# Optimization experiments

Hardware: AMD Instinct MI355X
Metric: run time of the kernel (lower is better)

The kernel has to match this reference:

```python
import jax, jax.numpy as jnp
import numpy as np

PAIRS = np.array([[0, 4], [1, 5], [2, 6], [3, 7], [0, 5], [1, 4], [2, 7], [3, 6]])


def setup_inputs() -> dict:
    key = jax.random.key(0)
    ks = jax.random.split(key, 40)
    rn = lambda k, shape: (jax.random.normal(k, shape, jnp.float32) * 0.05)
    inp = {
        "waiting": jax.random.uniform(ks[0], (1, 8), jnp.float32),
        "phase": jax.random.uniform(ks[1], (1, 8), jnp.float32),
        "wtime_mu": jax.random.uniform(ks[2], (1, 8), jnp.float32),
        "wtime_sigma": jax.random.uniform(ks[3], (1, 8), jnp.float32),
        "wtime_max": jax.random.uniform(ks[4], (1, 8), jnp.float32),
        "i_position": jax.random.uniform(ks[5], (1, 1), jnp.float32),
        "j_position": jax.random.uniform(ks[6], (1, 1), jnp.float32),
        # NN_demand: 14 -> 256 -> 32 -> 4
        "d_w1": rn(ks[7], (256, 14)), "d_b1": rn(ks[8], (256,)),
        "d_w2": rn(ks[9], (32, 256)), "d_b2": rn(ks[10], (32,)),
        "d_w3": rn(ks[11], (4, 32)), "d_b3": rn(ks[12], (4,)),
        # NN_coupled_demand: 8 -> 128 -> 32 -> 4
        "c_w1": rn(ks[13], (128, 8)), "c_b1": rn(ks[14], (128,)),
        "c_w2": rn(ks[15], (32, 128)), "c_b2": rn(ks[16], (32,)),
        "c_w3": rn(ks[17], (4, 32)), "c_b3": rn(ks[18], (4,)),
        # Conv_D: 1x1 convs 8 -> 256 -> 32 -> 2
        "dD_w1": rn(ks[19], (256, 8)), "dD_b1": rn(ks[20], (256,)),
        "dD_w2": rn(ks[21], (32, 256)), "dD_b2": rn(ks[22], (32,)),
        "dD_w3": rn(ks[23], (2, 32)), "dD_b3": rn(ks[24], (2,)),
        # Conv_C: 1x1 convs 3 -> 256 -> 32 -> 8, then (1,7) conv 8 -> 1
        "cC_w1": rn(ks[25], (256, 3)), "cC_b1": rn(ks[26], (256,)),
        "cC_w2": rn(ks[27], (32, 256)), "cC_b2": rn(ks[28], (32,)),
        "cC_w3": rn(ks[29], (8, 32)), "cC_b3": rn(ks[30], (8,)),
        "cC_w4": rn(ks[31], (8, 7)), "cC_b4": rn(ks[32], (1,)),
    }
    return inp


def _mlp3(x, w1, b1, w2, b2, w3, b3):
    h = jax.nn.relu(x @ w1.T + b1)
    h = jax.nn.relu(h @ w2.T + b2)
    return h @ w3.T + b3


def _frap_forward(waiting, phase, wtime_mu, wtime_sigma, wtime_max, i_position, j_position,
                  d_w1, d_b1, d_w2, d_b2, d_w3, d_b3,
                  c_w1, c_b1, c_w2, c_b2, c_w3, c_b3,
                  dD_w1, dD_b1, dD_w2, dD_b2, dD_w3, dD_b3,
                  cC_w1, cC_b1, cC_w2, cC_b2, cC_w3, cC_b3, cC_w4, cC_b4):
    pairs = jnp.asarray(PAIRS)
    # per-lane demand features: (8, 14) = [i, j, mu_l, sigma_l, max_l, wait_l, phase(8)]
    feat = jnp.concatenate([
        jnp.broadcast_to(i_position[0], (8, 1)),
        jnp.broadcast_to(j_position[0], (8, 1)),
        wtime_mu[0, :, None], wtime_sigma[0, :, None],
        wtime_max[0, :, None], waiting[0, :, None],
        jnp.broadcast_to(phase[0][None, :], (8, 8)),
    ], axis=1)
    demand = _mlp3(feat, d_w1, d_b1, d_w2, d_b2, d_w3, d_b3)  # (8, 4)
    # coupled demand per phase pair: (8, 8) -> (8, 4)
    vec = jnp.concatenate([demand[pairs[:, 0]], demand[pairs[:, 1]]], axis=1)
    dp = _mlp3(vec, c_w1, c_b1, c_w2, c_b2, c_w3, c_b3)  # (8, 4)
    # D tensor (8, 8, 7): D[0:4, i, k] = dp[i]; D[4:8, i, k] = dp[j(k)], j(k)=k + (k>=i)
    k = jnp.arange(7)
    i = jnp.arange(8)
    j_idx = k[None, :] + (k[None, :] >= i[:, None]).astype(jnp.int32)  # (8, 7)
    top = jnp.broadcast_to(dp.T[:, :, None], (4, 8, 7))
    bot = jnp.transpose(dp[j_idx], (2, 0, 1))  # (4, 8, 7)
    D = jnp.concatenate([top, bot], axis=0)  # (8, 8, 7)
    # Conv_D: 1x1 convs are channel matmuls on (C, H, W)
    h = jax.nn.relu(jnp.einsum('oc,chw->ohw', dD_w1, D) + dD_b1[:, None, None])
    h = jax.nn.relu(jnp.einsum('oc,chw->ohw', dD_w2, h) + dD_b2[:, None, None])
    H_d = jnp.einsum('oc,chw->ohw', dD_w3, h) + dD_b3[:, None, None]  # (2, 8, 7)
    comp = jnp.zeros((1, 8, 7), H_d.dtype)
    H_c = jnp.concatenate([H_d, comp], axis=0)  # (3, 8, 7)
    # Conv_C
    h = jax.nn.relu(jnp.einsum('oc,chw->ohw', cC_w1, H_c) + cC_b1[:, None, None])
    h = jax.nn.relu(jnp.einsum('oc,chw->ohw', cC_w2, h) + cC_b2[:, None, None])
    h = jax.nn.relu(jnp.einsum('oc,chw->ohw', cC_w3, h) + cC_b3[:, None, None])  # (8, 8, 7)
    # conv4: kernel (1,7), out (1, 8, 1); return C[0, :, 0] -> (8,)
    out = jnp.einsum('cw,chw->h', cC_w4, h) + cC_b4[0]
    return out


def reference(waiting, phase, wtime_mu, wtime_sigma, wtime_max, i_position, j_position,
              d_w1, d_b1, d_w2, d_b2, d_w3, d_b3,
              c_w1, c_b1, c_w2, c_b2, c_w3, c_b3,
              dD_w1, dD_b1, dD_w2, dD_b2, dD_w3, dD_b3,
              cC_w1, cC_b1, cC_w2, cC_b2, cC_w3, cC_b3, cC_w4, cC_b4):
    return _frap_forward(waiting, phase, wtime_mu, wtime_sigma, wtime_max, i_position, j_position,
                         d_w1, d_b1, d_w2, d_b2, d_w3, d_b3,
                         c_w1, c_b1, c_w2, c_b2, c_w3, c_b3,
                         dD_w1, dD_b1, dD_w2, dD_b2, dD_w3, dD_b3,
                         cC_w1, cC_b1, cC_w2, cC_b2, cC_w3, cC_b3, cC_w4, cC_b4)
```

## Files before the change

### kernel.cpp

```cpp
#include <hip/hip_runtime.h>


#define DEV __device__ __forceinline__

#define WAVE_SYNC() do { \
    asm volatile("s_waitcnt lgkmcnt(0)" ::: "memory"); \
    __builtin_amdgcn_sched_barrier(0); \
} while (0)

DEV float dot4a(float acc, float4 a, float4 b) {
    acc = fmaf(a.x, b.x, acc);
    acc = fmaf(a.y, b.y, acc);
    acc = fmaf(a.z, b.z, acc);
    acc = fmaf(a.w, b.w, acc);
    return acc;
}

DEV float warm_arr(const float* __restrict__ p, int n4, int id, float sink) {
    const float4* p4 = (const float4*)p;
    for (int i = id; i < n4; i += 448) {
        float4 v = p4[i];
        sink += v.x + v.y + v.z + v.w;
    }
    return sink;
}

DEV void conv_h2_vec(const float* __restrict__ big, const float* __restrict__ w2g,
                     const float* __restrict__ b2g, float* __restrict__ mid, int t)
{
    int wv = t >> 6;
    int ln = t & 63;
    int sl = ln & 15;
    int ch = wv * 4 + (ln >> 4);
    if (sl < 14) {
        const float4* wp = (const float4*)(w2g + ch * 256);
        const float* hrow = big + (sl << 8);
        int sw = sl & 7;
        float a0 = 0.0f, a1 = 0.0f, a2 = 0.0f, a3 = 0.0f;
#pragma unroll 4
        for (int g = 0; g < 64; g += 4) {
            float4 w0 = wp[g + 0], w1 = wp[g + 1], w2 = wp[g + 2], w3 = wp[g + 3];
            float4 h0 = *(const float4*)(hrow + (((g + 0) ^ sw) << 2));
            float4 h1 = *(const float4*)(hrow + (((g + 1) ^ sw) << 2));
            float4 h2 = *(const float4*)(hrow + (((g + 2) ^ sw) << 2));
            float4 h3v = *(const float4*)(hrow + (((g + 3) ^ sw) << 2));
            a0 = dot4a(a0, h0, w0);
            a1 = dot4a(a1, h1, w1);
            a2 = dot4a(a2, h2, w2);
            a3 = dot4a(a3, h3v, w3);
        }
        float r = ((a0 + a1) + (a2 + a3)) + b2g[ch];
        mid[ch * 14 + sl] = fmaxf(r, 0.0f);
    }
}

__global__ __launch_bounds__(512, 1) void frap_kernel(
    const float* __restrict__ waiting, const float* __restrict__ phase,
    const float* __restrict__ wtime_mu, const float* __restrict__ wtime_sigma,
    const float* __restrict__ wtime_max,
    const float* __restrict__ i_pos, const float* __restrict__ j_pos,
    const float* __restrict__ d_w1, const float* __restrict__ d_b1,
    const float* __restrict__ d_w2, const float* __restrict__ d_b2,
    const float* __restrict__ d_w3, const float* __restrict__ d_b3,
    const float* __restrict__ c_w1, const float* __restrict__ c_b1,
    const float* __restrict__ c_w2, const float* __restrict__ c_b2,
    const float* __restrict__ c_w3, const float* __restrict__ c_b3,
    const float* __restrict__ dD_w1, const float* __restrict__ dD_b1,
    const float* __restrict__ dD_w2, const float* __restrict__ dD_b2,
    const float* __restrict__ dD_w3, const float* __restrict__ dD_b3,
    const float* __restrict__ cC_w1, const float* __restrict__ cC_b1,
    const float* __restrict__ cC_w2, const float* __restrict__ cC_b2,
    const float* __restrict__ cC_w3, const float* __restrict__ cC_b3,
    const float* __restrict__ cC_w4, const float* __restrict__ cC_b4,
    float* __restrict__ out)
{
    __shared__ __align__(16) float sm[4096];
    const int t  = threadIdx.x;
    const int wg = blockIdx.x;
    const int ln = t & 63;

    float* feat16 = sm;
    float* dh1  = sm + 128;
    float* dh2  = sm + 2176;
    float* dem  = sm + 2432;
    float* ch1  = sm + 2464;
    float* ch2  = sm + 3488;
    float* big  = sm;
    float* mid  = sm + 3584;
    float* dp   = sm + 4032;
    float* Hd   = sm + 4064;
    float* h3   = sm;

    if (t < 64) {
        for (int rep = 0; rep < 2; ++rep) {
            int idx = rep * 64 + ln;
            int l = idx >> 4, c = idx & 15;
            float v = 0.0f;
            if      (c == 0) v = i_pos[0];
            else if (c == 1) v = j_pos[0];
            else if (c == 2) v = wtime_mu[l];
            else if (c == 3) v = wtime_sigma[l];
            else if (c == 4) v = wtime_max[l];
            else if (c == 5) v = waiting[l];
            else if (c < 14) v = phase[c - 6];
            feat16[idx] = v;
        }
        WAVE_SYNC();

        for (int q = 0; q < 4; ++q) {
            int o = q * 64 + ln;
            const float* w = d_w1 + o * 14;
            float w0 = w[0], w1 = w[1], w2 = w[2], w3 = w[3], w4 = w[4];
            float w5 = w[5], w6 = w[6], w7 = w[7], w8 = w[8], w9 = w[9];
            float wa = w[10], wb = w[11], wc = w[12], wd = w[13];
            float bias = d_b1[o];
#pragma unroll
            for (int l = 0; l < 8; ++l) {
                const float4* f4 = (const float4*)(feat16 + l * 16);
                float4 f0 = f4[0], f1 = f4[1], f2 = f4[2], f3 = f4[3];
                float acc = bias;
                acc = fmaf(f0.x, w0, acc); acc = fmaf(f0.y, w1, acc);
                acc = fmaf(f0.z, w2, acc); acc = fmaf(f0.w, w3, acc);
                acc = fmaf(f1.x, w4, acc); acc = fmaf(f1.y, w5, acc);
                acc = fmaf(f1.z, w6, acc); acc = fmaf(f1.w, w7, acc);
                acc = fmaf(f2.x, w8, acc); acc = fmaf(f2.y, w9, acc);
                acc = fmaf(f2.z, wa, acc); acc = fmaf(f2.w, wb, acc);
                acc = fmaf(f3.x, wc, acc); acc = fmaf(f3.y, wd, acc);
                dh1[l * 256 + o] = fmaxf(acc, 0.0f);
            }
        }
        WAVE_SYNC();

        {
            int o = ln & 31, lh = ln >> 5;
            float acc0 = 0.0f, acc1 = 0.0f, acc2 = 0.0f, acc3 = 0.0f;
            const float4* w4p = (const float4*)(d_w2 + o * 256);
#pragma unroll 4
            for (int cb = 0; cb < 64; ++cb) {
                float4 w = w4p[cb];
                float4 h0 = *(const float4*)(dh1 + (lh * 4 + 0) * 256 + cb * 4);
                float4 h1 = *(const float4*)(dh1 + (lh * 4 + 1) * 256 + cb * 4);
                float4 h2 = *(const float4*)(dh1 + (lh * 4 + 2) * 256 + cb * 4);
                float4 h3v = *(const float4*)(dh1 + (lh * 4 + 3) * 256 + cb * 4);
                acc0 = dot4a(acc0, h0, w);
                acc1 = dot4a(acc1, h1, w);
                acc2 = dot4a(acc2, h2, w);
                acc3 = dot4a(acc3, h3v, w);
            }
            float b = d_b2[o];
            dh2[(lh * 4 + 0) * 32 + o] = fmaxf(acc0 + b, 0.0f);
            dh2[(lh * 4 + 1) * 32 + o] = fmaxf(acc1 + b, 0.0f);
            dh2[(lh * 4 + 2) * 32 + o] = fmaxf(acc2 + b, 0.0f);
            dh2[(lh * 4 + 3) * 32 + o] = fmaxf(acc3 + b, 0.0f);
        }
        WAVE_SYNC();

        if (ln < 32) {
            int l = ln >> 2, o = ln & 3;
            const float4* w = (const float4*)(d_w3 + o * 32);
            const float4* h = (const float4*)(dh2 + l * 32);
            float acc = d_b3[o];
#pragma unroll
            for (int g = 0; g < 8; ++g) acc = dot4a(acc, h[g], w[g]);
            dem[ln] = acc;
        }
        WAVE_SYNC();

        for (int rep = 0; rep < 2; ++rep) {
            int o = rep * 64 + ln;
            const float4* w = (const float4*)(c_w1 + o * 8);
            float4 w0 = w[0], w1 = w[1];
            float bias = c_b1[o];
#pragma unroll
            for (int p = 0; p < 8; ++p) {
                int a0 = p & 3;
                int a1 = (p < 4) ? (4 + (p & 3)) : (4 + ((p & 3) ^ 1));
                float4 va = *(const float4*)(dem + a0 * 4);
                float4 vb = *(const float4*)(dem + a1 * 4);
                float acc = dot4a(dot4a(bias, va, w0), vb, w1);
                ch1[p * 128 + o] = fmaxf(acc, 0.0f);
            }
        }
        WAVE_SYNC();

        {
            int o = ln & 31, lh = ln >> 5;
            float acc0 = 0.0f, acc1 = 0.0f, acc2 = 0.0f, acc3 = 0.0f;
            const float4* w4p = (const float4*)(c_w2 + o * 128);
#pragma unroll 4
            for (int cb = 0; cb < 32; ++cb) {
                float4 w = w4p[cb];
                float4 h0 = *(const float4*)(ch1 + (lh * 4 + 0) * 128 + cb * 4);
                float4 h1 = *(const float4*)(ch1 + (lh * 4 + 1) * 128 + cb * 4);
                float4 h2 = *(const float4*)(ch1 + (lh * 4 + 2) * 128 + cb * 4);
                float4 h3v = *(const float4*)(ch1 + (lh * 4 + 3) * 128 + cb * 4);
                acc0 = dot4a(acc0, h0, w);
                acc1 = dot4a(acc1, h1, w);
                acc2 = dot4a(acc2, h2, w);
                acc3 = dot4a(acc3, h3v, w);
            }
            float b = c_b2[o];
            ch2[(lh * 4 + 0) * 32 + o] = fmaxf(acc0 + b, 0.0f);
            ch2[(lh * 4 + 1) * 32 + o] = fmaxf(acc1 + b, 0.0f);
            ch2[(lh * 4 + 2) * 32 + o] = fmaxf(acc2 + b, 0.0f);
            ch2[(lh * 4 + 3) * 32 + o] = fmaxf(acc3 + b, 0.0f);
        }
        WAVE_SYNC();

        if (ln < 32) {
            int l = ln >> 2, o = ln & 3;
            const float4* w = (const float4*)(c_w3 + o * 32);
            const float4* h = (const float4*)(ch2 + l * 32);
            float acc = c_b3[o];
#pragma unroll
            for (int g = 0; g < 8; ++g) acc = dot4a(acc, h[g], w[g]);
            dp[ln] = acc;
        }
    } else {
        int id = t - 64;
        float snk = 0.0f;
        snk = warm_arr(d_w1,  896, id, snk);
        snk = warm_arr(d_b1,   64, id, snk);
        snk = warm_arr(d_w2, 2048, id, snk);
        snk = warm_arr(d_b2,    8, id, snk);
        snk = warm_arr(d_w3,   32, id, snk);
        snk = warm_arr(d_b3,    1, id, snk);
        snk = warm_arr(c_w1,  256, id, snk);
        snk = warm_arr(c_b1,   32, id, snk);
        snk = warm_arr(c_w2, 1024, id, snk);
        snk = warm_arr(c_b2,    8, id, snk);
        snk = warm_arr(c_w3,   32, id, snk);
        snk = warm_arr(c_b3,    1, id, snk);
        snk = warm_arr(dD_w1, 512, id, snk);
        snk = warm_arr(dD_b1,  64, id, snk);
        snk = warm_arr(dD_w2, 2048, id, snk);
        snk = warm_arr(dD_b2,   8, id, snk);
        snk = warm_arr(dD_w3,  16, id, snk);
        snk = warm_arr(cC_w1, 192, id, snk);
        snk = warm_arr(cC_b1,  64, id, snk);
        snk = warm_arr(cC_w2, 2048, id, snk);
        snk = warm_arr(cC_b2,   8, id, snk);
        snk = warm_arr(cC_w3,  64, id, snk);
        snk = warm_arr(cC_b3,   2, id, snk);
        snk = warm_arr(cC_w4,  14, id, snk);
        asm volatile("" :: "v"(snk));
    }
    __syncthreads();

    {
        const float4* dp4 = (const float4*)dp;
        int o = t & 255;
        const float4* wrow = (const float4*)(dD_w1 + o * 8);
        float4 w0 = wrow[0], w1 = wrow[1];
        float bias = dD_b1[o];
#pragma unroll
        for (int it = 0; it < 7; ++it) {
            int sl = (t >> 8) + it * 2;
            int sg = wg * 14 + sl;
            int i = sg / 7, k = sg - i * 7;
            int j = k + (k >= i ? 1 : 0);
            float acc = dot4a(dot4a(bias, dp4[i], w0), dp4[j], w1);
            big[(sl << 8) + (o ^ ((sl & 7) << 2))] = fmaxf(acc, 0.0f);
        }
    }
    __syncthreads();

    conv_h2_vec(big, dD_w2, dD_b2, mid, t);
    __syncthreads();

    if (t < 112) {
        int kq = t & 3, u = t >> 2;
        int o = (u >= 14) ? 1 : 0;
        int s = u - o * 14;
        float acc = 0.0f;
#pragma unroll
        for (int cc = 0; cc < 8; ++cc) {
            int c = kq * 8 + cc;
            acc = fmaf(mid[c * 14 + s], dD_w3[o * 32 + c], acc);
        }
        acc += __shfl_xor(acc, 1);
        acc += __shfl_xor(acc, 2);
        if (kq == 0) Hd[o * 14 + s] = acc + dD_b3[o];
    }
    __syncthreads();

    {
        int o = t & 255;
        float w0 = cC_w1[o * 3], w1 = cC_w1[o * 3 + 1];
        float bias = cC_b1[o];
#pragma unroll
        for (int it = 0; it < 7; ++it) {
            int sl = (t >> 8) + it * 2;
            float acc = fmaf(Hd[14 + sl], w1, fmaf(Hd[sl], w0, bias));
            big[(sl << 8) + (o ^ ((sl & 7) << 2))] = fmaxf(acc, 0.0f);
        }
    }
    __syncthreads();

    conv_h2_vec(big, cC_w2, cC_b2, mid, t);
    __syncthreads();

    if (t < 448) {
        int kq = t & 3, u = t >> 2;
        int o = u & 7, s = u >> 3;
        float acc = 0.0f;
#pragma unroll
        for (int cc = 0; cc < 8; ++cc) {
            int c = kq * 8 + cc;
            acc = fmaf(mid[c * 14 + s], cC_w3[o * 32 + c], acc);
        }
        acc += __shfl_xor(acc, 1);
        acc += __shfl_xor(acc, 2);
        if (kq == 0) h3[o * 14 + s] = fmaxf(acc + cC_b3[o], 0.0f);
    }
    __syncthreads();

    if (t < 16) {
        int r = t >> 3, c = t & 7;
        float p = 0.0f;
#pragma unroll
        for (int w = 0; w < 7; ++w)
            p = fmaf(cC_w4[c * 7 + w], h3[c * 14 + r * 7 + w], p);
#pragma unroll
        for (int off = 1; off < 8; off <<= 1) p += __shfl_xor(p, off);
        if (c == 0) out[wg * 2 + r] = p + cC_b4[0];
    }
}

extern "C" void kernel_launch(void* const* d_in, const int* in_sizes, int n_in,
                              void* d_out, int out_size, void* d_ws, size_t ws_size,
                              hipStream_t stream) {
    (void)in_sizes; (void)n_in; (void)d_ws; (void)ws_size; (void)out_size;
    const float* a[33];
    for (int i = 0; i < 33; ++i) a[i] = (const float*)d_in[i];
    frap_kernel<<<dim3(4), dim3(512), 0, stream>>>(
        a[0], a[1], a[2], a[3], a[4], a[5], a[6],
        a[7], a[8], a[9], a[10], a[11], a[12],
        a[13], a[14], a[15], a[16], a[17], a[18],
        a[19], a[20], a[21], a[22], a[23], a[24],
        a[25], a[26], a[27], a[28], a[29], a[30], a[31], a[32],
        (float*)d_out);
}
```

Measured before the change: 27.88 us.

## Split work across eight blocks and spread demand MLP over all threads

The grid goes from 4 to 8 workgroups, so each block computes one output row of 7 spatial positions instead of two rows of 14. The first two layers of the demand MLP, which a single wave used to run, are now spread over all 512 threads using split-K with shuffle reductions. The conv layer-2 routine is also rewritten with a two-way K split. This cuts the serial single-wave prologue and the per-block conv work, at the cost of extra block-wide barriers and the redundant prologue running in twice as many blocks.

```diff
diff --git a/kernel.cpp b/kernel.cpp
--- a/kernel.cpp
+++ b/kernel.cpp
@@ -28,30 +28,31 @@
 DEV void conv_h2_vec(const float* __restrict__ big, const float* __restrict__ w2g,
                      const float* __restrict__ b2g, float* __restrict__ mid, int t)
 {
-    int wv = t >> 6;
-    int ln = t & 63;
-    int sl = ln & 15;
-    int ch = wv * 4 + (ln >> 4);
-    if (sl < 14) {
-        const float4* wp = (const float4*)(w2g + ch * 256);
+    int kq = t & 1;
+    int u  = t >> 1;
+    int ch = u >> 3, sl = u & 7;
+    float a0 = 0.0f, a1 = 0.0f, a2 = 0.0f, a3 = 0.0f;
+    if (sl < 7) {
+        const float4* wp = (const float4*)(w2g + ch * 256) + kq * 32;
         const float* hrow = big + (sl << 8);
-        int sw = sl & 7;
-        float a0 = 0.0f, a1 = 0.0f, a2 = 0.0f, a3 = 0.0f;
-#pragma unroll 4
-        for (int g = 0; g < 64; g += 4) {
+#pragma unroll 2
+        for (int g = 0; g < 32; g += 4) {
+            int gg = kq * 32 + g;
             float4 w0 = wp[g + 0], w1 = wp[g + 1], w2 = wp[g + 2], w3 = wp[g + 3];
-            float4 h0 = *(const float4*)(hrow + (((g + 0) ^ sw) << 2));
-            float4 h1 = *(const float4*)(hrow + (((g + 1) ^ sw) << 2));
-            float4 h2 = *(const float4*)(hrow + (((g + 2) ^ sw) << 2));
-            float4 h3v = *(const float4*)(hrow + (((g + 3) ^ sw) << 2));
+            float4 h0 = *(const float4*)(hrow + (((gg + 0) ^ sl) << 2));
+            float4 h1 = *(const float4*)(hrow + (((gg + 1) ^ sl) << 2));
+            float4 h2 = *(const float4*)(hrow + (((gg + 2) ^ sl) << 2));
+            float4 h3v = *(const float4*)(hrow + (((gg + 3) ^ sl) << 2));
             a0 = dot4a(a0, h0, w0);
             a1 = dot4a(a1, h1, w1);
             a2 = dot4a(a2, h2, w2);
             a3 = dot4a(a3, h3v, w3);
         }
-        float r = ((a0 + a1) + (a2 + a3)) + b2g[ch];
-        mid[ch * 14 + sl] = fmaxf(r, 0.0f);
-    }
+    }
+    float r = (a0 + a1) + (a2 + a3);
+    r += __shfl_xor(r, 1);
+    if (sl < 7 && kq == 0)
+        mid[ch * 7 + sl] = fmaxf(r + b2g[ch], 0.0f);
 }
 
 __global__ __launch_bounds__(512, 1) void frap_kernel(
@@ -86,9 +87,9 @@
     float* ch1  = sm + 2464;
     float* ch2  = sm + 3488;
     float* big  = sm;
-    float* mid  = sm + 3584;
-    float* dp   = sm + 4032;
-    float* Hd   = sm + 4064;
+    float* mid  = sm + 3744;
+    float* dp   = sm + 3968;
+    float* Hd   = sm + 4000;
     float* h3   = sm;
 
     if (t < 64) {
@@ -104,117 +105,6 @@
             else if (c == 5) v = waiting[l];
             else if (c < 14) v = phase[c - 6];
             feat16[idx] = v;
-        }
-        WAVE_SYNC();
-
-        for (int q = 0; q < 4; ++q) {
-            int o = q * 64 + ln;
-            const float* w = d_w1 + o * 14;
-            float w0 = w[0], w1 = w[1], w2 = w[2], w3 = w[3], w4 = w[4];
-            float w5 = w[5], w6 = w[6], w7 = w[7], w8 = w[8], w9 = w[9];
-            float wa = w[10], wb = w[11], wc = w[12], wd = w[13];
-            float bias = d_b1[o];
-#pragma unroll
-            for (int l = 0; l < 8; ++l) {
-                const float4* f4 = (const float4*)(feat16 + l * 16);
-                float4 f0 = f4[0], f1 = f4[1], f2 = f4[2], f3 = f4[3];
-                float acc = bias;
-                acc = fmaf(f0.x, w0, acc); acc = fmaf(f0.y, w1, acc);
-                acc = fmaf(f0.z, w2, acc); acc = fmaf(f0.w, w3, acc);
-                acc = fmaf(f1.x, w4, acc); acc = fmaf(f1.y, w5, acc);
-                acc = fmaf(f1.z, w6, acc); acc = fmaf(f1.w, w7, acc);
-                acc = fmaf(f2.x, w8, acc); acc = fmaf(f2.y, w9, acc);
-                acc = fmaf(f2.z, wa, acc); acc = fmaf(f2.w, wb, acc);
-                acc = fmaf(f3.x, wc, acc); acc = fmaf(f3.y, wd, acc);
-                dh1[l * 256 + o] = fmaxf(acc, 0.0f);
-            }
-        }
-        WAVE_SYNC();
-
-        {
-            int o = ln & 31, lh = ln >> 5;
-            float acc0 = 0.0f, acc1 = 0.0f, acc2 = 0.0f, acc3 = 0.0f;
-            const float4* w4p = (const float4*)(d_w2 + o * 256);
-#pragma unroll 4
-            for (int cb = 0; cb < 64; ++cb) {
-                float4 w = w4p[cb];
-                float4 h0 = *(const float4*)(dh1 + (lh * 4 + 0) * 256 + cb * 4);
-                float4 h1 = *(const float4*)(dh1 + (lh * 4 + 1) * 256 + cb * 4);
-                float4 h2 = *(const float4*)(dh1 + (lh * 4 + 2) * 256 + cb * 4);
-                float4 h3v = *(const float4*)(dh1 + (lh * 4 + 3) * 256 + cb * 4);
-                acc0 = dot4a(acc0, h0, w);
-                acc1 = dot4a(acc1, h1, w);
-                acc2 = dot4a(acc2, h2, w);
-                acc3 = dot4a(acc3, h3v, w);
-            }
-            float b = d_b2[o];
-            dh2[(lh * 4 + 0) * 32 + o] = fmaxf(acc0 + b, 0.0f);
-            dh2[(lh * 4 + 1) * 32 + o] = fmaxf(acc1 + b, 0.0f);
-            dh2[(lh * 4 + 2) * 32 + o] = fmaxf(acc2 + b, 0.0f);
-            dh2[(lh * 4 + 3) * 32 + o] = fmaxf(acc3 + b, 0.0f);
-        }
-        WAVE_SYNC();
-
-        if (ln < 32) {
-            int l = ln >> 2, o = ln & 3;
-            const float4* w = (const float4*)(d_w3 + o * 32);
-            const float4* h = (const float4*)(dh2 + l * 32);
-            float acc = d_b3[o];
-#pragma unroll
-            for (int g = 0; g < 8; ++g) acc = dot4a(acc, h[g], w[g]);
-            dem[ln] = acc;
-        }
-        WAVE_SYNC();
-
-        for (int rep = 0; rep < 2; ++rep) {
-            int o = rep * 64 + ln;
-            const float4* w = (const float4*)(c_w1 + o * 8);
-            float4 w0 = w[0], w1 = w[1];
-            float bias = c_b1[o];
-#pragma unroll
-            for (int p = 0; p < 8; ++p) {
-                int a0 = p & 3;
-                int a1 = (p < 4) ? (4 + (p & 3)) : (4 + ((p & 3) ^ 1));
-                float4 va = *(const float4*)(dem + a0 * 4);
-                float4 vb = *(const float4*)(dem + a1 * 4);
-                float acc = dot4a(dot4a(bias, va, w0), vb, w1);
-                ch1[p * 128 + o] = fmaxf(acc, 0.0f);
-            }
-        }
-        WAVE_SYNC();
-
-        {
-            int o = ln & 31, lh = ln >> 5;
-            float acc0 = 0.0f, acc1 = 0.0f, acc2 = 0.0f, acc3 = 0.0f;
-            const float4* w4p = (const float4*)(c_w2 + o * 128);
-#pragma unroll 4
-            for (int cb = 0; cb < 32; ++cb) {
-                float4 w = w4p[cb];
-                float4 h0 = *(const float4*)(ch1 + (lh * 4 + 0) * 128 + cb * 4);
-                float4 h1 = *(const float4*)(ch1 + (lh * 4 + 1) * 128 + cb * 4);
-                float4 h2 = *(const float4*)(ch1 + (lh * 4 + 2) * 128 + cb * 4);
-                float4 h3v = *(const float4*)(ch1 + (lh * 4 + 3) * 128 + cb * 4);
-                acc0 = dot4a(acc0, h0, w);
-                acc1 = dot4a(acc1, h1, w);
-                acc2 = dot4a(acc2, h2, w);
-                acc3 = dot4a(acc3, h3v, w);
-            }
-            float b = c_b2[o];
-            ch2[(lh * 4 + 0) * 32 + o] = fmaxf(acc0 + b, 0.0f);
-            ch2[(lh * 4 + 1) * 32 + o] = fmaxf(acc1 + b, 0.0f);
-            ch2[(lh * 4 + 2) * 32 + o] = fmaxf(acc2 + b, 0.0f);
-            ch2[(lh * 4 + 3) * 32 + o] = fmaxf(acc3 + b, 0.0f);
-        }
-        WAVE_SYNC();
-
-        if (ln < 32) {
-            int l = ln >> 2, o = ln & 3;
-            const float4* w = (const float4*)(c_w3 + o * 32);
-            const float4* h = (const float4*)(ch2 + l * 32);
-            float acc = c_b3[o];
-#pragma unroll
-            for (int g = 0; g < 8; ++g) acc = dot4a(acc, h[g], w[g]);
-            dp[ln] = acc;
         }
     } else {
         int id = t - 64;
@@ -247,20 +137,112 @@
     }
     __syncthreads();
 
+    for (int q = 0; q < 4; ++q) {
+        int idx = t + q * 512;
+        int l = idx >> 8, o = idx & 255;
+        const float* w = d_w1 + o * 14;
+        const float* f = feat16 + l * 16;
+        float acc = d_b1[o];
+#pragma unroll
+        for (int c = 0; c < 14; ++c) acc = fmaf(f[c], w[c], acc);
+        dh1[idx] = fmaxf(acc, 0.0f);
+    }
+    __syncthreads();
+
+    {
+        int kq = t & 1;
+        int u  = t >> 1;
+        int l = u >> 5, o = u & 31;
+        const float4* w = (const float4*)(d_w2 + o * 256) + kq * 32;
+        const float4* h = (const float4*)(dh1 + l * 256) + kq * 32;
+        float acc = 0.0f;
+#pragma unroll 4
+        for (int g = 0; g < 32; ++g) acc = dot4a(acc, h[g], w[g]);
+        acc += __shfl_xor(acc, 1);
+        if (kq == 0) dh2[l * 32 + o] = fmaxf(acc + d_b2[o], 0.0f);
+    }
+    __syncthreads();
+
+    if (t < 64) {
+        if (ln < 32) {
+            int l = ln >> 2, o = ln & 3;
+            const float4* w = (const float4*)(d_w3 + o * 32);
+            const float4* h = (const float4*)(dh2 + l * 32);
+            float acc = d_b3[o];
+#pragma unroll
+            for (int g = 0; g < 8; ++g) acc = dot4a(acc, h[g], w[g]);
+            dem[ln] = acc;
+        }
+        WAVE_SYNC();
+
+        for (int rep = 0; rep < 2; ++rep) {
+            int o = rep * 64 + ln;
+            const float4* w = (const float4*)(c_w1 + o * 8);
+            float4 w0 = w[0], w1 = w[1];
+            float bias = c_b1[o];
+#pragma unroll
+            for (int p = 0; p < 8; ++p) {
+                int a0 = p & 3;
+                int a1 = (p < 4) ? (4 + (p & 3)) : (4 + ((p & 3) ^ 1));
+                float4 va = *(const float4*)(dem + a0 * 4);
+                float4 vb = *(const float4*)(dem + a1 * 4);
+                float acc = dot4a(dot4a(bias, va, w0), vb, w1);
+                ch1[p * 128 + o] = fmaxf(acc, 0.0f);
+            }
+        }
+        WAVE_SYNC();
+
+        {
+            int o = ln & 31, lh = ln >> 5;
+            float acc0 = 0.0f, acc1 = 0.0f, acc2 = 0.0f, acc3 = 0.0f;
+            const float4* w4p = (const float4*)(c_w2 + o * 128);
+#pragma unroll 4
+            for (int cb = 0; cb < 32; ++cb) {
+                float4 w = w4p[cb];
+                float4 h0 = *(const float4*)(ch1 + (lh * 4 + 0) * 128 + cb * 4);
+                float4 h1 = *(const float4*)(ch1 + (lh * 4 + 1) * 128 + cb * 4);
+                float4 h2 = *(const float4*)(ch1 + (lh * 4 + 2) * 128 + cb * 4);
+                float4 h3v = *(const float4*)(ch1 + (lh * 4 + 3) * 128 + cb * 4);
+                acc0 = dot4a(acc0, h0, w);
+                acc1 = dot4a(acc1, h1, w);
+                acc2 = dot4a(acc2, h2, w);
+                acc3 = dot4a(acc3, h3v, w);
+            }
+            float b = c_b2[o];
+            ch2[(lh * 4 + 0) * 32 + o] = fmaxf(acc0 + b, 0.0f);
+            ch2[(lh * 4 + 1) * 32 + o] = fmaxf(acc1 + b, 0.0f);
+            ch2[(lh * 4 + 2) * 32 + o] = fmaxf(acc2 + b, 0.0f);
+            ch2[(lh * 4 + 3) * 32 + o] = fmaxf(acc3 + b, 0.0f);
+        }
+        WAVE_SYNC();
+
+        if (ln < 32) {
+            int l = ln >> 2, o = ln & 3;
+            const float4* w = (const float4*)(c_w3 + o * 32);
+            const float4* h = (const float4*)(ch2 + l * 32);
+            float acc = c_b3[o];
+#pragma unroll
+            for (int g = 0; g < 8; ++g) acc = dot4a(acc, h[g], w[g]);
+            dp[ln] = acc;
+        }
+    }
+    __syncthreads();
+
     {
         const float4* dp4 = (const float4*)dp;
         int o = t & 255;
         const float4* wrow = (const float4*)(dD_w1 + o * 8);
         float4 w0 = wrow[0], w1 = wrow[1];
         float bias = dD_b1[o];
-#pragma unroll
-        for (int it = 0; it < 7; ++it) {
+        float4 di = dp4[wg];
+#pragma unroll
+        for (int it = 0; it < 4; ++it) {
             int sl = (t >> 8) + it * 2;
-            int sg = wg * 14 + sl;
-            int i = sg / 7, k = sg - i * 7;
-            int j = k + (k >= i ? 1 : 0);
-            float acc = dot4a(dot4a(bias, dp4[i], w0), dp4[j], w1);
-            big[(sl << 8) + (o ^ ((sl & 7) << 2))] = fmaxf(acc, 0.0f);
+            if (sl < 7) {
+                int j = sl + (sl >= wg ? 1 : 0);
+                float acc = dot4a(dot4a(bias, di, w0), dp4[j], w1);
+                big[(sl << 8) + (((o >> 2) ^ sl) << 2) + (o & 3)] = fmaxf(acc, 0.0f);
+            }
         }
     }
     __syncthreads();
@@ -268,19 +250,19 @@
     conv_h2_vec(big, dD_w2, dD_b2, mid, t);
     __syncthreads();
 
-    if (t < 112) {
+    if (t < 56) {
         int kq = t & 3, u = t >> 2;
-        int o = (u >= 14) ? 1 : 0;
-        int s = u - o * 14;
+        int o = (u >= 7) ? 1 : 0;
+        int s = u - o * 7;
         float acc = 0.0f;
 #pragma unroll
         for (int cc = 0; cc < 8; ++cc) {
             int c = kq * 8 + cc;
-            acc = fmaf(mid[c * 14 + s], dD_w3[o * 32 + c], acc);
+            acc = fmaf(mid[c * 7 + s], dD_w3[o * 32 + c], acc);
         }
         acc += __shfl_xor(acc, 1);
         acc += __shfl_xor(acc, 2);
-        if (kq == 0) Hd[o * 14 + s] = acc + dD_b3[o];
+        if (kq == 0) Hd[o * 7 + s] = acc + dD_b3[o];
     }
     __syncthreads();
 
@@ -289,10 +271,12 @@
         float w0 = cC_w1[o * 3], w1 = cC_w1[o * 3 + 1];
         float bias = cC_b1[o];
 #pragma unroll
-        for (int it = 0; it < 7; ++it) {
+        for (int it = 0; it < 4; ++it) {
             int sl = (t >> 8) + it * 2;
-            float acc = fmaf(Hd[14 + sl], w1, fmaf(Hd[sl], w0, bias));
-            big[(sl << 8) + (o ^ ((sl & 7) << 2))] = fmaxf(acc, 0.0f);
+            if (sl < 7) {
+                float acc = fmaf(Hd[7 + sl], w1, fmaf(Hd[sl], w0, bias));
+                big[(sl << 8) + (((o >> 2) ^ sl) << 2) + (o & 3)] = fmaxf(acc, 0.0f);
+            }
         }
     }
     __syncthreads();
@@ -300,30 +284,30 @@
     conv_h2_vec(big, cC_w2, cC_b2, mid, t);
     __syncthreads();
 
-    if (t < 448) {
+    if (t < 224) {
         int kq = t & 3, u = t >> 2;
         int o = u & 7, s = u >> 3;
         float acc = 0.0f;
 #pragma unroll
         for (int cc = 0; cc < 8; ++cc) {
             int c = kq * 8 + cc;
-            acc = fmaf(mid[c * 14 + s], cC_w3[o * 32 + c], acc);
+            acc = fmaf(mid[c * 7 + s], cC_w3[o * 32 + c], acc);
         }
         acc += __shfl_xor(acc, 1);
         acc += __shfl_xor(acc, 2);
-        if (kq == 0) h3[o * 14 + s] = fmaxf(acc + cC_b3[o], 0.0f);
-    }
-    __syncthreads();
-
-    if (t < 16) {
-        int r = t >> 3, c = t & 7;
+        if (kq == 0) h3[o * 7 + s] = fmaxf(acc + cC_b3[o], 0.0f);
+    }
+    __syncthreads();
+
+    if (t < 64) {
         float p = 0.0f;
-#pragma unroll
-        for (int w = 0; w < 7; ++w)
-            p = fmaf(cC_w4[c * 7 + w], h3[c * 14 + r * 7 + w], p);
-#pragma unroll
-        for (int off = 1; off < 8; off <<= 1) p += __shfl_xor(p, off);
-        if (c == 0) out[wg * 2 + r] = p + cC_b4[0];
+        if (ln < 56) {
+            int c = ln / 7, w = ln % 7;
+            p = cC_w4[c * 7 + w] * h3[c * 7 + w];
+        }
+#pragma unroll
+        for (int off = 1; off < 64; off <<= 1) p += __shfl_xor(p, off);
+        if (ln == 0) out[wg] = p + cC_b4[0];
     }
 }
 
@@ -333,7 +317,7 @@
     (void)in_sizes; (void)n_in; (void)d_ws; (void)ws_size; (void)out_size;
     const float* a[33];
     for (int i = 0; i < 33; ++i) a[i] = (const float*)d_in[i];
-    frap_kernel<<<dim3(4), dim3(512), 0, stream>>>(
+    frap_kernel<<<dim3(8), dim3(512), 0, stream>>>(
         a[0], a[1], a[2], a[3], a[4], a[5], a[6],
         a[7], a[8], a[9], a[10], a[11], a[12],
         a[13], a[14], a[15], a[16], a[17], a[18],
```

Measured after the change: 34.24 us. 1.23x slower.
